# Optimization experiments

Measured on AMD Instinct MI355X. Metric: run time of the kernel, lower is better.

Reference implementation:

```python
import math
import jax, jax.numpy as jnp
import numpy as np

B, N, QN, LN = 2, 2048, 512, 256
D, QD, LD = 1024, 1024, 64
H, QH = 16, 16
HD, QHD = D // H, QD // QH


def setup_inputs() -> dict:
    key = jax.random.key(0)
    ks = jax.random.split(key, 12)
    g = lambda k, shp, s: (jax.random.normal(k, shp, dtype=jnp.float32) * s)
    return {
        "x": g(ks[0], (B, N, D), 1.0),
        "query": g(ks[1], (B, QN, QD), 1.0),
        "low_res": g(ks[2], (B, LN, LD), 1.0),
        "W_qkv": g(ks[3], (D, 3 * D), 0.02),          # self.qkv (no bias)
        "W_xkv": g(ks[4], (D, 2 * QD), 0.02),         # self.x_to_query_kv
        "W_qlin": g(ks[5], (QD, 3 * QD), 0.02),       # self.query_linear
        "gate": g(ks[6], (1, QH, 1, 1), 0.5),         # self.gate
        "W_proj": g(ks[7], (D, D), 0.02),
        "b_proj": jnp.zeros((D,), jnp.float32),
        "W_qproj": g(ks[8], (QD, QD), 0.02),
        "b_qproj": jnp.zeros((QD,), jnp.float32),
        "W_lrproj": g(ks[9], (LD, LD), 0.02),
        "b_lrproj": jnp.zeros((LD,), jnp.float32),
    }


def _sdpa(q, k, v):
    # q,k,v: [B, H, S, hd]; plain softmax attention, no mask, no dropout
    scale = 1.0 / math.sqrt(q.shape[-1])
    attn = jax.nn.softmax(jnp.einsum("bhqd,bhkd->bhqk", q, k) * scale, axis=-1)
    return jnp.einsum("bhqk,bhkd->bhqd", attn, v)


def reference(x, query, low_res, W_qkv, W_xkv, W_qlin, gate,
              W_proj, b_proj, W_qproj, b_qproj, W_lrproj, b_lrproj):
    # --- self-attention over x ---
    qkv = (x @ W_qkv).reshape(B, N, 3, H, HD).transpose(2, 0, 3, 1, 4)
    q, k, v = qkv[0], qkv[1], qkv[2]          # [B,H,N,HD]
    x_attn = _sdpa(q, k, v)                    # [B,H,N,HD]

    # --- zero_init gated cross-attention for query stream ---
    kv = (x @ W_xkv).reshape(B, N, 2, QH, QHD).transpose(2, 0, 3, 1, 4)
    k2, v2 = kv[0], kv[1]                      # [B,QH,N,QHD]
    qqkv = (query @ W_qlin).reshape(B, QN, 3, QH, QHD).transpose(2, 0, 3, 1, 4)
    qq, qk, qv = qqkv[0], qqkv[1], qqkv[2]     # [B,QH,QN,QHD]

    xk = jnp.concatenate([k2, qk], axis=2)     # [B,QH,N+QN,QHD]
    xv = jnp.concatenate([v2, qv], axis=2)
    scale = 1.0 / math.sqrt(QHD)
    scores = jnp.einsum("bhqd,bhkd->bhqk", qq, xk) * scale  # [B,QH,QN,N+QN]
    # split softmax with learned tanh gate on the x segment
    attn = jnp.concatenate(
        [jnp.tanh(gate) * jax.nn.softmax(scores[..., :N], axis=-1),
         jax.nn.softmax(scores[..., N:], axis=-1)], axis=-1)
    q_attn = jnp.einsum("bhqk,bhkd->bhqd", attn, xv)  # [B,QH,QN,QHD]

    # --- output projections ---
    x_out = x_attn.transpose(0, 2, 1, 3).reshape(B, N, D) @ W_proj + b_proj
    query_out = q_attn.transpose(0, 2, 1, 3).reshape(B, QN, QD) @ W_qproj + b_qproj
    # faithful to source: low_res passes through unmodified in zero_init branch,
    # then transpose(1,2)+reshape scramble, then proj
    lr_out = jnp.swapaxes(low_res, 1, 2).reshape(B, LN, LD) @ W_lrproj + b_lrproj
    return (x_out, query_out, lr_out)
```

## Files before the change

kernel.cpp:

```cpp
#include <hip/hip_runtime.h>

typedef __bf16 bf16;
typedef __bf16 bf16x4 __attribute__((ext_vector_type(4)));
typedef __bf16 bf16x8 __attribute__((ext_vector_type(8)));
typedef float  f32x4  __attribute__((ext_vector_type(4)));


#define AS1(p) ((const __attribute__((address_space(1))) void*)(p))
#define AS3(p) ((__attribute__((address_space(3))) void*)(p))
__device__ __forceinline__ void gl16(const void* g, void* l) {
    __builtin_amdgcn_global_load_lds(AS1(g), AS3(l), 16, 0, 0);
}
#define BAR_VM4() asm volatile("s_waitcnt vmcnt(4)\n\ts_barrier" ::: "memory")
#define BAR_VM2() asm volatile("s_waitcnt vmcnt(2)\n\ts_barrier" ::: "memory")
#define BAR_VM0() asm volatile("s_waitcnt vmcnt(0)\n\ts_barrier" ::: "memory")
#define BAR()     asm volatile("s_barrier" ::: "memory")

__global__ __launch_bounds__(256) void prep(
    const float* __restrict__ x, bf16* __restrict__ xb,
    const float* __restrict__ query, bf16* __restrict__ qryb,
    const float* __restrict__ W_qkv, const float* __restrict__ W_xkv,
    const float* __restrict__ W_qlin, const float* __restrict__ W_proj,
    const float* __restrict__ W_qproj,
    bf16* __restrict__ WtX, bf16* __restrict__ Wtqlin,
    bf16* __restrict__ Wtproj, bf16* __restrict__ Wtqproj,
    const float* __restrict__ lowres, const float* __restrict__ W_lr,
    const float* __restrict__ b_lr, float* __restrict__ lrout)
{
    __shared__ float T[64][65];
    const int bid = blockIdx.x, tid = threadIdx.x;

    if (bid < 2560) {
        int idx = (bid * 256 + tid) << 3;
        const float* s; bf16* d;
        if (idx < 4194304) { s = x + idx; d = xb + idx; }
        else { int k = idx - 4194304; s = query + k; d = qryb + k; }
        f32x4 a = *(const f32x4*)s, c = *(const f32x4*)(s + 4);
        bf16x8 v;
#pragma unroll
        for (int j = 0; j < 4; j++) { v[j] = (bf16)a[j]; v[4 + j] = (bf16)c[j]; }
        *(bf16x8*)d = v;
    } else if (bid < 5120) {
        int w = bid - 2560;
        int gx = w % 160, k0 = (w / 160) << 6;
        const float* S; bf16* D; int N;
        if (gx < 48)       { S = W_qkv;   D = WtX;     N = 3072; }
        else if (gx < 80)  { S = W_xkv;   D = WtX + (size_t)3072 * 1024; N = 2048; gx -= 48; }
        else if (gx < 128) { S = W_qlin;  D = Wtqlin;  N = 3072; gx -= 80; }
        else if (gx < 144) { S = W_proj;  D = Wtproj;  N = 1024; gx -= 128; }
        else               { S = W_qproj; D = Wtqproj; N = 1024; gx -= 144; }
        int n0 = gx << 6;
#pragma unroll
        for (int rr = 0; rr < 4; rr++) {
            int row = (rr << 4) + (tid >> 4), col = (tid & 15) << 2;
            f32x4 v = *(const f32x4*)(S + (size_t)(k0 + row) * N + n0 + col);
#pragma unroll
            for (int j = 0; j < 4; j++) T[col + j][row] = v[j];
        }
        __syncthreads();
        {
            int n = tid >> 2, kc = (tid & 3) << 4;
            bf16x8 v0, v1;
#pragma unroll
            for (int j = 0; j < 8; j++) {
                v0[j] = (bf16)T[n][kc + j];
                v1[j] = (bf16)T[n][kc + 8 + j];
            }
            bf16* dp = D + (size_t)(n0 + n) * 1024 + k0 + kc;
            *(bf16x8*)dp = v0; *(bf16x8*)(dp + 8) = v1;
        }
    } else {
        int idx = (bid - 5120) * 256 + tid;
        int j = idx & 63, i = (idx >> 6) & 255, b = idx >> 14;
        float acc = b_lr[j];
        const float* lr = lowres + ((size_t)b << 14);
        for (int k = 0; k < 64; k++) {
            int f = i * 64 + k;
            acc += lr[((f & 255) << 6) + (f >> 8)] * W_lr[(k << 6) + j];
        }
        lrout[idx] = acc;
    }
}

template <int NSPLIT, typename OT>
__device__ __forceinline__ void gemm_core(
    bf16* gsm,
    const bf16* __restrict__ A, const bf16* __restrict__ Bt,
    OT* __restrict__ C0, OT* __restrict__ C1, OT* __restrict__ C2,
    OT* __restrict__ C3, OT* __restrict__ C4,
    const float* __restrict__ bias, int N, int K, int tshift,
    float s0scale, unsigned vmask, int bx, int by)
{
    const int tid  = threadIdx.x;
    const int wave = tid >> 6, lane = tid & 63;
    const int l15  = lane & 15, g = lane >> 4;
    const int wr   = wave & 1, wc = wave >> 1;
    const int m0   = by << 7, n0 = bx << 7;

    f32x4 acc[4][4] = {};

    auto stage = [&](int t, int bsel) {
        const bf16* Ab = A  + (size_t)m0 * K + (t << 5);
        const bf16* Bb = Bt + (size_t)n0 * K + (t << 5);
        char* Ad = (char*)gsm + (bsel << 14);
        char* Bd = Ad + 8192;
        const int wb = (tid & 192) << 4;
#pragma unroll
        for (int i = 0; i < 2; i++) {
            int L = (i << 8) + tid;
            int r = L >> 2, c = (L & 3) ^ ((r ^ (r >> 2)) & 3);
            gl16(Ab + (size_t)r * K + (c << 3), Ad + (i << 12) + wb);
            gl16(Bb + (size_t)r * K + (c << 3), Bd + (i << 12) + wb);
        }
    };
    auto compute = [&](int bsel) {
        const char* Ad = (const char*)gsm + (bsel << 14);
        const char* Bd = Ad + 8192;
        bf16x8 af[4], bq[4];
#pragma unroll
        for (int mb = 0; mb < 4; mb++) {
            int row = (wr << 6) + (mb << 4) + l15;
            af[mb] = *(const bf16x8*)(Ad + (row << 6)
                      + ((g ^ ((row ^ (row >> 2)) & 3)) << 4));
        }
#pragma unroll
        for (int nb = 0; nb < 4; nb++) {
            int row = (wc << 6) + (nb << 4) + l15;
            bq[nb] = *(const bf16x8*)(Bd + (row << 6)
                      + ((g ^ ((row ^ (row >> 2)) & 3)) << 4));
        }
#pragma unroll
        for (int mb = 0; mb < 4; mb++)
#pragma unroll
            for (int nb = 0; nb < 4; nb++)
                acc[mb][nb] = __builtin_amdgcn_mfma_f32_16x16x32_bf16(
                    af[mb], bq[nb], acc[mb][nb], 0, 0, 0);
    };

    const int T = K >> 5;
    stage(0, 0);
    for (int t = 0; t < T; t++) {
        int bsel = t & 1;
        if (t + 1 < T) { stage(t + 1, bsel ^ 1); BAR_VM4(); }
        else           { BAR_VM0(); }
        compute(bsel);
        BAR();
    }

    if constexpr (NSPLIT == 0) {
#pragma unroll
        for (int mb = 0; mb < 4; mb++)
#pragma unroll
            for (int nb = 0; nb < 4; nb++) {
                int n = n0 + (wc << 6) + (nb << 4) + l15;
                int mbase = m0 + (wr << 6) + (mb << 4) + (g << 2);
                float bi = bias[n];
#pragma unroll
                for (int r = 0; r < 4; r++)
                    C0[(size_t)(mbase + r) * N + n] = (OT)(acc[mb][nb][r] + bi);
            }
    } else {
        BAR();
        bf16* stg = gsm + wave * 4608;
        const int nh = (n0 >> 6) + wc;
        const int sl = nh >> 4, hq = nh & 15;
        const float scl = (sl == 0) ? s0scale : 1.0f;
        const bool isv = (vmask >> sl) & 1;
        if (isv) {
#pragma unroll
            for (int mb = 0; mb < 4; mb++)
#pragma unroll
                for (int nb = 0; nb < 4; nb++)
#pragma unroll
                    for (int r = 0; r < 4; r++)
                        stg[((nb << 4) + l15) * 72 + (mb << 4) + (g << 2) + r]
                            = (bf16)(acc[mb][nb][r] * scl);
        } else {
#pragma unroll
            for (int mb = 0; mb < 4; mb++)
#pragma unroll
                for (int nb = 0; nb < 4; nb++)
#pragma unroll
                    for (int r = 0; r < 4; r++)
                        stg[((mb << 4) + (g << 2) + r) << 6 | ((nb << 4) + l15)]
                            = (bf16)(acc[mb][nb][r] * scl);
        }
        __syncthreads();
        const int ntok = 1 << tshift;
        const int tok0 = m0 + (wr << 6);
        const int b = tok0 >> tshift, t0 = tok0 & (ntok - 1);
        const int bh_ = (b << 4) + hq;
        OT* dst = (sl == 0) ? C0 : (sl == 1) ? C1 : (sl == 2) ? C2
                : (sl == 3) ? C3 : C4;
#pragma unroll
        for (int rr = 0; rr < 8; rr++) {
            int idx = (rr << 6) + lane;
            int rowi = idx >> 3, c = idx & 7;
            if (isv) {
                bf16x8 vv = *(const bf16x8*)&stg[rowi * 72 + (c << 3)];
                bf16x4 lo, hi;
#pragma unroll
                for (int jj = 0; jj < 4; jj++) { lo[jj] = vv[jj]; hi[jj] = vv[4 + jj]; }
                int tb = t0 + ((c >> 2) << 5);
                int gamma0 = (c << 1) & 7;
                int p_lo = (((gamma0 & 3) << 1) + (gamma0 >> 2)) << 2;
                size_t base = ((size_t)((bh_ << 6) + rowi)) * ntok + tb;
                *(bf16x4*)&dst[base + p_lo] = lo;
                *(bf16x4*)&dst[base + p_lo + 8] = hi;
            } else {
                bf16x8 vv = *(const bf16x8*)&stg[(rowi << 6) + (c << 3)];
                *(bf16x8*)&dst[(((size_t)bh_ * ntok + t0 + rowi) << 6) + (c << 3)] = vv;
            }
        }
    }
}

__global__ __launch_bounds__(256) void gemm_qkv(
    const bf16* __restrict__ A0, const bf16* __restrict__ Bt0,
    bf16* __restrict__ qb, bf16* __restrict__ kb, bf16* __restrict__ vbt,
    bf16* __restrict__ k2, bf16* __restrict__ v2t,
    const bf16* __restrict__ A1, const bf16* __restrict__ Bt1,
    bf16* __restrict__ qq, bf16* __restrict__ qk, bf16* __restrict__ qvt,
    float sc2)
{
    __shared__ __align__(16) bf16 gsm[18432];
    int idx = blockIdx.x;
    const bf16 *A, *Bt; bf16 *C0, *C1, *C2, *C3, *C4;
    int N, tshift, bx, by; unsigned vmask;
    if (idx < 1280) {
        A = A0; Bt = Bt0; C0 = qb; C1 = kb; C2 = vbt; C3 = k2; C4 = v2t;
        N = 5120; tshift = 11; vmask = 0b10100u; bx = idx % 40; by = idx / 40;
    } else {
        idx -= 1280;
        A = A1; Bt = Bt1; C0 = qq; C1 = qk; C2 = qvt; C3 = nullptr; C4 = nullptr;
        N = 3072; tshift = 9; vmask = 0b100u; bx = idx % 24; by = idx / 24;
    }
    gemm_core<1, bf16>(gsm, A, Bt, C0, C1, C2, C3, C4, nullptr,
                       N, 1024, tshift, sc2, vmask, bx, by);
}

__global__ __launch_bounds__(256) void gemm_proj(
    const bf16* __restrict__ ax, const bf16* __restrict__ Wtp,
    float* __restrict__ o0, const float* __restrict__ bp,
    const bf16* __restrict__ aq, const bf16* __restrict__ Wtq,
    float* __restrict__ o1, const float* __restrict__ bq)
{
    __shared__ __align__(16) bf16 gsm[18432];
    int idx = blockIdx.x;
    const bf16 *A, *Bt; float* C; const float* bias; int bx, by;
    if (idx < 256) { A = ax; Bt = Wtp; C = o0; bias = bp; bx = idx & 7; by = idx >> 3; }
    else { idx -= 256; A = aq; Bt = Wtq; C = o1; bias = bq; bx = idx & 7; by = idx >> 3; }
    gemm_core<0, float>(gsm, A, Bt, C, nullptr, nullptr, nullptr, nullptr, bias,
                        1024, 1024, 0, 1.0f, 0u, bx, by);
}

__global__ __launch_bounds__(256) void flash3m(
    const bf16* __restrict__ Q1, const bf16* __restrict__ K1,
    const bf16* __restrict__ V1t, bf16* __restrict__ O1,
    const bf16* __restrict__ Q2, const bf16* __restrict__ K2a,
    const bf16* __restrict__ V2at, const bf16* __restrict__ K2b,
    const bf16* __restrict__ V2bt, bf16* __restrict__ O2,
    const float* __restrict__ gate)
{
    __shared__ __align__(16) bf16 fsm[8704];

    const int tid = threadIdx.x;
    const int wave = tid >> 6, lane = tid & 63;
    const int l15 = lane & 15, g = lane >> 4;

    const int j = blockIdx.x & 7, i = blockIdx.x >> 3;
    const bf16 *Qp, *Ka, *Vat, *Kb2, *Vbt2; bf16* Op;
    int nq, nk1, nk2, q0, bh;
    bool cross;
    if (i < 16) {
        cross = true;
        bh = (j << 2) + (i >> 2); q0 = (i & 3) << 7;
        Qp = Q2; Ka = K2a; Vat = V2at; Kb2 = K2b; Vbt2 = V2bt; Op = O2;
        nq = 512; nk1 = 2048; nk2 = 512;
    } else {
        cross = false;
        int is = i - 16;
        bh = (j << 2) + (is >> 4); q0 = (is & 15) << 7;
        Qp = Q1; Ka = K1; Vat = V1t; Kb2 = nullptr; Vbt2 = nullptr; Op = O1;
        nq = 2048; nk1 = 2048; nk2 = 0;
    }
    const int h = bh & 15, b = bh >> 4;
    const int T1 = nk1 >> 5, T = T1 + (cross ? (nk2 >> 5) : 0);

    bf16x8 qf[2][2];
#pragma unroll
    for (int qb = 0; qb < 2; qb++) {
        const bf16* qrow = Qp + ((size_t)bh * nq + q0 + (wave << 5) + (qb << 4) + l15) * 64;
        qf[qb][0] = *(const bf16x8*)(qrow + (g << 3));
        qf[qb][1] = *(const bf16x8*)(qrow + 32 + (g << 3));
    }

    f32x4 Oacc[4][2] = {}, Ofin[4][2] = {};
    float lcur[2] = {0.0f, 0.0f};
    const float gmul = cross ? tanhf(gate[h]) : 1.0f;

    auto stage = [&](int t, int bsel) {
        const bf16 *kb, *vb; int stride;
        if (!cross || t < T1) {
            kb = Ka + ((size_t)bh * nk1 + (t << 5)) * 64;
            vb = Vat + ((size_t)bh << 6) * nk1 + (t << 5);
            stride = nk1;
        } else {
            int u = t - T1;
            kb = Kb2 + ((size_t)bh * nk2 + (u << 5)) * 64;
            vb = Vbt2 + ((size_t)bh << 6) * nk2 + (u << 5);
            stride = nk2;
        }
        char* Kd = (char*)fsm + (bsel << 12);
        char* Vd = (char*)fsm + 8192 + (bsel << 12);
        const int wb = (tid & 192) << 4;
        {
            int r = tid >> 3, c = (tid & 7) ^ (r & 7);
            gl16(kb + (r << 6) + (c << 3), Kd + wb);
        }
        {
            int r = tid >> 2, c = (tid & 3) ^ (r & 3);
            gl16(vb + (size_t)r * stride + (c << 3), Vd + wb);
        }
    };

    auto compute = [&](int t, int bsel) {
        const char* Kb = (const char*)fsm + (bsel << 12);
        const char* Vb = (const char*)fsm + 8192 + (bsel << 12);
        f32x4 S[2][2];
#pragma unroll
        for (int nb = 0; nb < 2; nb++) {
            int row = (nb << 4) + l15;
            bf16x8 kf0 = *(const bf16x8*)(Kb + (row << 7) + ((g ^ (row & 7)) << 4));
            bf16x8 kf1 = *(const bf16x8*)(Kb + (row << 7) + (((4 + g) ^ (row & 7)) << 4));
#pragma unroll
            for (int qb = 0; qb < 2; qb++) {
                f32x4 s = {};
                s = __builtin_amdgcn_mfma_f32_16x16x32_bf16(kf0, qf[qb][0], s, 0, 0, 0);
                s = __builtin_amdgcn_mfma_f32_16x16x32_bf16(kf1, qf[qb][1], s, 0, 0, 0);
                S[nb][qb] = s;
            }
        }
        bf16x8 pf[2];
#pragma unroll
        for (int qb = 0; qb < 2; qb++) {
            float rs = 0.0f;
#pragma unroll
            for (int r = 0; r < 4; r++) {
                float p0 = __builtin_amdgcn_exp2f(S[0][qb][r]);
                float p1 = __builtin_amdgcn_exp2f(S[1][qb][r]);
                rs += p0 + p1;
                pf[qb][r] = (bf16)p0;
                pf[qb][4 + r] = (bf16)p1;
            }
            lcur[qb] += rs;
        }
#pragma unroll
        for (int hb = 0; hb < 4; hb++) {
            int row = (hb << 4) + l15;
            bf16x8 vf = *(const bf16x8*)(Vb + (row << 6) + ((g ^ (row & 3)) << 4));
#pragma unroll
            for (int qb = 0; qb < 2; qb++)
                Oacc[hb][qb] = __builtin_amdgcn_mfma_f32_16x16x32_bf16(
                    vf, pf[qb], Oacc[hb][qb], 0, 0, 0);
        }
        if (cross && t == T1 - 1) {
#pragma unroll
            for (int qb = 0; qb < 2; qb++) {
                float l = lcur[qb];
                l += __shfl_xor(l, 16);
                l += __shfl_xor(l, 32);
                float w = gmul / l;
#pragma unroll
                for (int hb = 0; hb < 4; hb++)
#pragma unroll
                    for (int r = 0; r < 4; r++) {
                        Ofin[hb][qb][r] += Oacc[hb][qb][r] * w;
                        Oacc[hb][qb][r] = 0.0f;
                    }
                lcur[qb] = 0.0f;
            }
        }
    };

    stage(0, 0);
    for (int t = 0; t < T; t++) {
        int bsel = t & 1;
        if (t + 1 < T) { stage(t + 1, bsel ^ 1); BAR_VM2(); }
        else           { BAR_VM0(); }
        compute(t, bsel);
        BAR();
    }

    float wfin[2];
#pragma unroll
    for (int qb = 0; qb < 2; qb++) {
        float l = lcur[qb];
        l += __shfl_xor(l, 16);
        l += __shfl_xor(l, 32);
        wfin[qb] = 1.0f / l;
    }

    bf16* OB = fsm;
#pragma unroll
    for (int hb = 0; hb < 4; hb++)
#pragma unroll
        for (int qb = 0; qb < 2; qb++)
#pragma unroll
            for (int r = 0; r < 4; r++) {
                float v = Oacc[hb][qb][r] * wfin[qb];
                if (cross) v += Ofin[hb][qb][r];
                OB[((hb << 4) + (g << 2) + r) * 136 + (wave << 5) + (qb << 4) + l15] = (bf16)v;
            }
    __syncthreads();
    {
        int q = tid >> 1, half = (tid & 1) << 5;
        bf16x8 o[4];
#pragma unroll
        for (int j2 = 0; j2 < 4; j2++)
#pragma unroll
            for (int jj = 0; jj < 8; jj++)
                o[j2][jj] = OB[(half + (j2 << 3) + jj) * 136 + q];
        bf16* op = Op + (((size_t)b * nq + q0 + q) << 10) + (h << 6) + half;
#pragma unroll
        for (int j2 = 0; j2 < 4; j2++)
            *(bf16x8*)(op + (j2 << 3)) = o[j2];
    }
}

extern "C" void kernel_launch(void* const* d_in, const int* in_sizes, int n_in,
                              void* d_out, int out_size, void* d_ws, size_t ws_size,
                              hipStream_t stream)
{
    const float* x       = (const float*)d_in[0];
    const float* query   = (const float*)d_in[1];
    const float* lowres  = (const float*)d_in[2];
    const float* W_qkv   = (const float*)d_in[3];
    const float* W_xkv   = (const float*)d_in[4];
    const float* W_qlin  = (const float*)d_in[5];
    const float* gate    = (const float*)d_in[6];
    const float* W_proj  = (const float*)d_in[7];
    const float* b_proj  = (const float*)d_in[8];
    const float* W_qproj = (const float*)d_in[9];
    const float* b_qproj = (const float*)d_in[10];
    const float* W_lr    = (const float*)d_in[11];
    const float* b_lr    = (const float*)d_in[12];
    float* out = (float*)d_out;

    const float sc2 = 0.125f * 1.44269504088896f;

    char* ws = (char*)d_ws;
    bf16* WtX     = (bf16*)ws; ws += 10485760;
    bf16* Wtqlin  = (bf16*)ws; ws += 6291456;
    bf16* Wtproj  = (bf16*)ws; ws += 2097152;
    bf16* Wtqproj = (bf16*)ws; ws += 2097152;
    bf16* xb      = (bf16*)ws; ws += 8388608;
    bf16* qryb    = (bf16*)ws; ws += 2097152;
    bf16* qb      = (bf16*)ws; ws += 8388608;
    bf16* kb      = (bf16*)ws; ws += 8388608;
    bf16* vbt     = (bf16*)ws; ws += 8388608;
    bf16* k2      = (bf16*)ws; ws += 8388608;
    bf16* v2t     = (bf16*)ws; ws += 8388608;
    bf16* qq      = (bf16*)ws; ws += 2097152;
    bf16* qk      = (bf16*)ws; ws += 2097152;
    bf16* qvt     = (bf16*)ws; ws += 2097152;
    bf16* ax = xb;
    bf16* aq = qryb;

    prep<<<5248, 256, 0, stream>>>(
        x, xb, query, qryb, W_qkv, W_xkv, W_qlin, W_proj, W_qproj,
        WtX, Wtqlin, Wtproj, Wtqproj, lowres, W_lr, b_lr, out + 5242880);

    gemm_qkv<<<1472, 256, 0, stream>>>(
        xb, WtX, qb, kb, vbt, k2, v2t, qryb, Wtqlin, qq, qk, qvt, sc2);

    flash3m<<<640, 256, 0, stream>>>(
        qb, kb, vbt, ax, qq, k2, v2t, qk, qvt, aq, gate);

    gemm_proj<<<320, 256, 0, stream>>>(
        ax, Wtproj, out, b_proj, aq, Wtqproj, out + 4194304, b_qproj);

    (void)in_sizes; (void)n_in; (void)out_size; (void)ws_size;
}
```

Baseline: 296.1 us.

## Swizzle GEMM block order, use MFMA row sums, incrementalize flash staging addresses

```diff
diff --git a/kernel.cpp b/kernel.cpp
--- a/kernel.cpp
+++ b/kernel.cpp
@@ -224,7 +224,7 @@
     float sc2)
 {
     __shared__ __align__(16) bf16 gsm[18432];
-    int idx = blockIdx.x;
+    int idx = (blockIdx.x & 7) * 184 + (blockIdx.x >> 3);
     const bf16 *A, *Bt; bf16 *C0, *C1, *C2, *C3, *C4;
     int N, tshift, bx, by; unsigned vmask;
     if (idx < 1280) {
@@ -246,7 +246,7 @@
     float* __restrict__ o1, const float* __restrict__ bq)
 {
     __shared__ __align__(16) bf16 gsm[18432];
-    int idx = blockIdx.x;
+    int idx = (blockIdx.x & 7) * 40 + (blockIdx.x >> 3);
     const bf16 *A, *Bt; float* C; const float* bias; int bx, by;
     if (idx < 256) { A = ax; Bt = Wtp; C = o0; bias = bp; bx = idx & 7; by = idx >> 3; }
     else { idx -= 256; A = aq; Bt = Wtq; C = o1; bias = bq; bx = idx & 7; by = idx >> 3; }
@@ -295,33 +295,33 @@
         qf[qb][1] = *(const bf16x8*)(qrow + 32 + (g << 3));
     }
 
+    bf16x8 ones;
+#pragma unroll
+    for (int z = 0; z < 8; z++) ones[z] = (bf16)1.0f;
+
     f32x4 Oacc[4][2] = {}, Ofin[4][2] = {};
-    float lcur[2] = {0.0f, 0.0f};
+    f32x4 Lones[2] = {};
     const float gmul = cross ? tanhf(gate[h]) : 1.0f;
 
-    auto stage = [&](int t, int bsel) {
-        const bf16 *kb, *vb; int stride;
-        if (!cross || t < T1) {
-            kb = Ka + ((size_t)bh * nk1 + (t << 5)) * 64;
-            vb = Vat + ((size_t)bh << 6) * nk1 + (t << 5);
-            stride = nk1;
-        } else {
-            int u = t - T1;
-            kb = Kb2 + ((size_t)bh * nk2 + (u << 5)) * 64;
-            vb = Vbt2 + ((size_t)bh << 6) * nk2 + (u << 5);
-            stride = nk2;
+    const int kr = tid >> 3, kc = (tid & 7) ^ (kr & 7);
+    const int vr = tid >> 2, vc = (tid & 3) ^ (vr & 3);
+    const bf16* kaddr = Ka + ((size_t)bh * nk1) * 64 + (kr << 6) + (kc << 3);
+    const bf16* vaddr = Vat + ((size_t)bh << 6) * nk1 + (size_t)vr * nk1 + (vc << 3);
+    int staged = 0;
+
+    auto stage = [&](int bsel) {
+        if (cross && staged == T1) {
+            kaddr = Kb2 + ((size_t)bh * nk2) * 64 + (kr << 6) + (kc << 3);
+            vaddr = Vbt2 + ((size_t)bh << 6) * nk2 + (size_t)vr * nk2 + (vc << 3);
         }
         char* Kd = (char*)fsm + (bsel << 12);
         char* Vd = (char*)fsm + 8192 + (bsel << 12);
         const int wb = (tid & 192) << 4;
-        {
-            int r = tid >> 3, c = (tid & 7) ^ (r & 7);
-            gl16(kb + (r << 6) + (c << 3), Kd + wb);
-        }
-        {
-            int r = tid >> 2, c = (tid & 3) ^ (r & 3);
-            gl16(vb + (size_t)r * stride + (c << 3), Vd + wb);
-        }
+        gl16(kaddr, Kd + wb);
+        gl16(vaddr, Vd + wb);
+        kaddr += 2048;
+        vaddr += 32;
+        staged++;
     };
 
     auto compute = [&](int t, int bsel) {
@@ -343,18 +343,16 @@
         }
         bf16x8 pf[2];
 #pragma unroll
-        for (int qb = 0; qb < 2; qb++) {
-            float rs = 0.0f;
+        for (int qb = 0; qb < 2; qb++)
 #pragma unroll
             for (int r = 0; r < 4; r++) {
-                float p0 = __builtin_amdgcn_exp2f(S[0][qb][r]);
-                float p1 = __builtin_amdgcn_exp2f(S[1][qb][r]);
-                rs += p0 + p1;
-                pf[qb][r] = (bf16)p0;
-                pf[qb][4 + r] = (bf16)p1;
-            }
-            lcur[qb] += rs;
-        }
+                pf[qb][r]     = (bf16)__builtin_amdgcn_exp2f(S[0][qb][r]);
+                pf[qb][4 + r] = (bf16)__builtin_amdgcn_exp2f(S[1][qb][r]);
+            }
+#pragma unroll
+        for (int qb = 0; qb < 2; qb++)
+            Lones[qb] = __builtin_amdgcn_mfma_f32_16x16x32_bf16(
+                ones, pf[qb], Lones[qb], 0, 0, 0);
 #pragma unroll
         for (int hb = 0; hb < 4; hb++) {
             int row = (hb << 4) + l15;
@@ -367,10 +365,7 @@
         if (cross && t == T1 - 1) {
 #pragma unroll
             for (int qb = 0; qb < 2; qb++) {
-                float l = lcur[qb];
-                l += __shfl_xor(l, 16);
-                l += __shfl_xor(l, 32);
-                float w = gmul / l;
+                float w = gmul / Lones[qb][0];
 #pragma unroll
                 for (int hb = 0; hb < 4; hb++)
 #pragma unroll
@@ -378,15 +373,15 @@
                         Ofin[hb][qb][r] += Oacc[hb][qb][r] * w;
                         Oacc[hb][qb][r] = 0.0f;
                     }
-                lcur[qb] = 0.0f;
+                Lones[qb] = f32x4{};
             }
         }
     };
 
-    stage(0, 0);
+    stage(0);
     for (int t = 0; t < T; t++) {
         int bsel = t & 1;
-        if (t + 1 < T) { stage(t + 1, bsel ^ 1); BAR_VM2(); }
+        if (t + 1 < T) { stage(bsel ^ 1); BAR_VM2(); }
         else           { BAR_VM0(); }
         compute(t, bsel);
         BAR();
@@ -394,12 +389,8 @@
 
     float wfin[2];
 #pragma unroll
-    for (int qb = 0; qb < 2; qb++) {
-        float l = lcur[qb];
-        l += __shfl_xor(l, 16);
-        l += __shfl_xor(l, 32);
-        wfin[qb] = 1.0f / l;
-    }
+    for (int qb = 0; qb < 2; qb++)
+        wfin[qb] = (cross ? 1.0f : gmul) / Lones[qb][0];
 
     bf16* OB = fsm;
 #pragma unroll
```

After: 285.6 us. 1.04x faster.
